# Kernel optimization log

Measured on AMD Instinct MI355X. Metric: run time of the kernel, lower is better.

Reference implementation:

```python
import jax, jax.numpy as jnp
import numpy as np

SCALE = 56          # descriptor spatial size (self.scale)
K_POS = 3           # positives: softmin over 3 nearest prototypes


def setup_inputs() -> dict:
    key = jax.random.key(0)
    k1, k2, k3 = jax.random.split(key, 3)
    B, DIM, H, W_ = 4, 1792, SCALE, SCALE
    P = 3136  # num_prototypes
    p = jax.random.normal(k1, (B, DIM, H, W_), dtype=jnp.float32)
    W = jax.random.normal(k2, (DIM, DIM), dtype=jnp.float32) * (1.0 / np.sqrt(DIM))
    b = jnp.zeros((DIM,), dtype=jnp.float32)
    C = jax.random.normal(k3, (DIM, P), dtype=jnp.float32) * (1.0 / np.sqrt(DIM))
    return {"p": p, "W": W, "b": b, "C": C}


def reference(p, W, b, C):
    B, DIM, H, Wd = p.shape
    # Descriptor: 1x1 conv (CoordConv2d without coords), no sigmoid, no avg-pool
    phi = jnp.einsum('bchw,dc->bdhw', p, W) + b[None, :, None, None]
    # b c h w -> b (h w) c
    phi_p = jnp.transpose(phi.reshape(B, DIM, H * Wd), (0, 2, 1))  # [B, HW, D]
    # squared-distance trick: ||a||^2 + ||c||^2 - 2 a.c
    features = jnp.sum(phi_p * phi_p, axis=2, keepdims=True)       # [B, HW, 1]
    centers = jnp.sum(C * C, axis=0, keepdims=True)                # [1, P]
    f_c = 2.0 * jnp.matmul(phi_p, C)                               # [B, HW, P]
    dist = jnp.sqrt(features + centers - f_c)                      # [B, HW, P]
    # k smallest distances (ascending)
    d = -jax.lax.top_k(-dist, K_POS)[0]                            # [B, HW, K]
    # softmin weight of the nearest prototype times its distance
    w0 = jax.nn.softmax(-d, axis=-1)[:, :, 0]
    score_flat = (w0 * d[:, :, 0])[:, :, None]                     # [B, HW, 1]
    # b (h w) c -> b c h w
    score = jnp.transpose(score_flat.reshape(B, H, Wd, 1), (0, 3, 1, 2))
    return score
```

## Files before the change

### kernel.cpp

```cpp
#include <hip/hip_runtime.h>
#include <hip/hip_bf16.h>
#include <cfloat>

#define BATCH 4
#define DIMC 1792
#define HWSZ 3136
#define NPROT 3136
#define NPAD 3200
#define MROWS 12544

typedef unsigned short u16;
typedef unsigned int u32;
using bf16x8 = __attribute__((ext_vector_type(8))) short;
using f32x4  = __attribute__((ext_vector_type(4))) float;

__device__ __forceinline__ float bf2f(u32 u) { return __uint_as_float(u << 16); }
__device__ __forceinline__ u16 f2bf(float x) {
    __hip_bfloat16 h = __float2bfloat16(x);
    return *reinterpret_cast<u16*>(&h);
}

__device__ __forceinline__ void gload_lds16(const u16* g, u16* l) {
    __builtin_amdgcn_global_load_lds(
        (const __attribute__((address_space(1))) void*)g,
        (__attribute__((address_space(3))) void*)l, 16, 0, 0);
}

__device__ __forceinline__ void ins3(float v, float& t0, float& t1, float& t2) {
    if (v < t2) {
        if (v < t1) {
            t2 = t1;
            if (v < t0) { t1 = t0; t0 = v; }
            else        { t1 = v; }
        } else {
            t2 = v;
        }
    }
}

__global__ void pack_p_kernel(const float* __restrict__ p, u16* __restrict__ Pbf) {
    __shared__ float tile[32][33];
    int hw0 = blockIdx.x * 32, c0 = blockIdx.y * 32, b = blockIdx.z;
    int tx = threadIdx.x, ty = threadIdx.y;
#pragma unroll
    for (int j = 0; j < 32; j += 8)
        tile[ty + j][tx] = p[((size_t)(b * DIMC + c0 + ty + j)) * HWSZ + hw0 + tx];
    __syncthreads();
#pragma unroll
    for (int j = 0; j < 32; j += 8) {
        int r = b * HWSZ + hw0 + ty + j;
        Pbf[(size_t)r * DIMC + c0 + tx] = f2bf(tile[tx][ty + j]);
    }
}

__global__ void pack_w_kernel(const float* __restrict__ W, u16* __restrict__ Wbf) {
    size_t i = (size_t)(blockIdx.x * 256 + threadIdx.x) * 4;
    float4 v = *(const float4*)(W + i);
    ushort4 o;
    o.x = f2bf(v.x); o.y = f2bf(v.y); o.z = f2bf(v.z); o.w = f2bf(v.w);
    *(ushort4*)(Wbf + i) = o;
}

__global__ void pack_c_kernel(const float* __restrict__ C, u16* __restrict__ CTbf) {
    __shared__ float tile[32][33];
    int j0 = blockIdx.x * 32, d0 = blockIdx.y * 32;
    int tx = threadIdx.x, ty = threadIdx.y;
#pragma unroll
    for (int jj = 0; jj < 32; jj += 8)
        tile[ty + jj][tx] = C[(size_t)(d0 + ty + jj) * NPROT + j0 + tx];
    __syncthreads();
#pragma unroll
    for (int jj = 0; jj < 32; jj += 8)
        CTbf[(size_t)(j0 + ty + jj) * DIMC + d0 + tx] = f2bf(tile[tx][ty + jj]);
}

__global__ void cn_kernel(const float* __restrict__ C, float* __restrict__ cn) {
    int j  = blockIdx.x * 256 + threadIdx.x;
    int d0 = blockIdx.y * 128;
    if (j >= NPROT) return;
    float s = 0.f;
    for (int d = d0; d < d0 + 128; ++d) {
        float v = C[(size_t)d * NPROT + j];
        s += v * v;
    }
    atomicAdd(&cn[j], s);
}

template<bool BIAS>
__global__ __launch_bounds__(256) void gemm_kernel(
    const u16* __restrict__ A,
    const u16* __restrict__ B,
    const float* __restrict__ bias,
    u16* __restrict__ out, int ldo)
{
    __shared__ __align__(16) u16 Als[128 * 32];
    __shared__ __align__(16) u16 Bls[128 * 32];
    const int tid  = threadIdx.x;
    const int wid  = tid >> 6;
    const int lane = tid & 63;
    const int r0 = blockIdx.x * 128;
    const int n0 = blockIdx.y * 128;

    const int srow = lane >> 2;
    const int sseg = (lane & 3) * 8;
    const u16* Ag = A + (size_t)(r0 + wid * 32 + srow) * DIMC + sseg;
    const u16* Bg = B + (size_t)(n0 + wid * 32 + srow) * DIMC + sseg;
    u16* AlsW = Als + wid * 1024;
    u16* BlsW = Bls + wid * 1024;

    const int wm = (wid >> 1) * 64;
    const int wn = (wid & 1) * 64;
    const int lrow = lane & 15;
    const int kseg = (lane >> 4) * 8;
    const int rsub = (lane >> 4) * 4;

    f32x4 acc[4][4];
#pragma unroll
    for (int m = 0; m < 4; ++m)
#pragma unroll
        for (int n = 0; n < 4; ++n)
            acc[m][n] = (f32x4){0.f, 0.f, 0.f, 0.f};

    for (int k0 = 0; k0 < DIMC; k0 += 32) {
        gload_lds16(Ag + k0,                      AlsW);
        gload_lds16(Ag + (size_t)16 * DIMC + k0,  AlsW + 512);
        gload_lds16(Bg + k0,                      BlsW);
        gload_lds16(Bg + (size_t)16 * DIMC + k0,  BlsW + 512);
        __syncthreads();
        bf16x8 af[4], bv[4];
#pragma unroll
        for (int m = 0; m < 4; ++m)
            af[m] = *(const bf16x8*)(Als + (wm + m * 16 + lrow) * 32 + kseg);
#pragma unroll
        for (int n = 0; n < 4; ++n)
            bv[n] = *(const bf16x8*)(Bls + (wn + n * 16 + lrow) * 32 + kseg);
#pragma unroll
        for (int m = 0; m < 4; ++m)
#pragma unroll
            for (int n = 0; n < 4; ++n)
                acc[m][n] = __builtin_amdgcn_mfma_f32_16x16x32_bf16(
                    af[m], bv[n], acc[m][n], 0, 0, 0);
        __syncthreads();
    }

#pragma unroll
    for (int n = 0; n < 4; ++n) {
        int col = n0 + wn + n * 16 + lrow;
        float bs = 0.f;
        if (BIAS) bs = bias[col];
#pragma unroll
        for (int m = 0; m < 4; ++m) {
            f32x4 v = acc[m][n];
#pragma unroll
            for (int i = 0; i < 4; ++i) {
                int row = r0 + wm + m * 16 + rsub + i;
                out[(size_t)row * ldo + col] = f2bf(v[i] + bs);
            }
        }
    }
}

__global__ void rn_kernel(const u16* __restrict__ phibf, float* __restrict__ rn) {
    int row  = blockIdx.x * 4 + (threadIdx.x >> 6);
    int lane = threadIdx.x & 63;
    const u16* pr = phibf + (size_t)row * DIMC;
    float s = 0.f;
#pragma unroll
    for (int it = 0; it < 7; ++it) {
        uint2 v = *(const uint2*)(pr + (it * 64 + lane) * 4);
        float f0 = bf2f(v.x & 0xffffu), f1 = bf2f(v.x >> 16);
        float f2 = bf2f(v.y & 0xffffu), f3 = bf2f(v.y >> 16);
        s += f0 * f0 + f1 * f1 + f2 * f2 + f3 * f3;
    }
#pragma unroll
    for (int off = 32; off > 0; off >>= 1) s += __shfl_down(s, off);
    if (lane == 0) rn[row] = s;
}

__global__ void top3_final_kernel(const u16* __restrict__ fc,
                                  const float* __restrict__ cn,
                                  const float* __restrict__ rn,
                                  float* __restrict__ out) {
    int row  = blockIdx.x * 4 + (threadIdx.x >> 6);
    int lane = threadIdx.x & 63;
    const u16* fr = fc + (size_t)row * NPAD;
    float t0 = FLT_MAX, t1 = FLT_MAX, t2 = FLT_MAX;
#pragma unroll
    for (int it = 0; it < 6; ++it) {
        int j0 = (it * 64 + lane) * 8;
        uint4 v = *(const uint4*)(fr + j0);
        u32 wd[4] = {v.x, v.y, v.z, v.w};
#pragma unroll
        for (int e = 0; e < 4; ++e) {
            float flo = bf2f(wd[e] & 0xffffu);
            float fhi = bf2f(wd[e] >> 16);
            ins3(cn[j0 + 2 * e]     - 2.f * flo, t0, t1, t2);
            ins3(cn[j0 + 2 * e + 1] - 2.f * fhi, t0, t1, t2);
        }
    }
    {
        int j = 3072 + lane;
        ins3(cn[j] - 2.f * bf2f((u32)fr[j]), t0, t1, t2);
    }
#pragma unroll
    for (int off = 32; off > 0; off >>= 1) {
        float s0 = __shfl_xor(t0, off);
        float s1 = __shfl_xor(t1, off);
        float s2 = __shfl_xor(t2, off);
        ins3(s0, t0, t1, t2);
        ins3(s1, t0, t1, t2);
        ins3(s2, t0, t1, t2);
    }
    if (lane == 0) {
        float rv = rn[row];
        float d0 = sqrtf(rv + t0), d1 = sqrtf(rv + t1), d2 = sqrtf(rv + t2);
        float w0 = 1.f / (1.f + expf(d0 - d1) + expf(d0 - d2));
        out[row] = w0 * d0;
    }
}

extern "C" void kernel_launch(void* const* d_in, const int* in_sizes, int n_in,
                              void* d_out, int out_size, void* d_ws, size_t ws_size,
                              hipStream_t stream) {
    const float* p    = (const float*)d_in[0];
    const float* W    = (const float*)d_in[1];
    const float* bias = (const float*)d_in[2];
    const float* C    = (const float*)d_in[3];
    float* out = (float*)d_out;

    char* w = (char*)d_ws;
    u16* Pbf   = (u16*)w;  w += (size_t)MROWS * DIMC * 2;
    u16* Wbf   = (u16*)w;  w += (size_t)DIMC * DIMC * 2;
    u16* CTbf  = (u16*)w;  w += (size_t)NPAD * DIMC * 2;
    u16* phibf = (u16*)w;  w += (size_t)MROWS * DIMC * 2;
    u16* fc    = (u16*)w;  w += (size_t)MROWS * NPAD * 2;
    float* cn  = (float*)w; w += (size_t)NPROT * 4;
    float* rn  = (float*)w;

    hipMemsetAsync(cn, 0, NPROT * sizeof(float), stream);

    pack_p_kernel<<<dim3(HWSZ / 32, DIMC / 32, BATCH), dim3(32, 8), 0, stream>>>(p, Pbf);
    pack_w_kernel<<<(DIMC * DIMC / 4) / 256, 256, 0, stream>>>(W, Wbf);
    pack_c_kernel<<<dim3(NPROT / 32, DIMC / 32), dim3(32, 8), 0, stream>>>(C, CTbf);
    cn_kernel<<<dim3((NPROT + 255) / 256, DIMC / 128), 256, 0, stream>>>(C, cn);

    gemm_kernel<true><<<dim3(MROWS / 128, DIMC / 128), 256, 0, stream>>>(
        Pbf, Wbf, bias, phibf, DIMC);
    rn_kernel<<<MROWS / 4, 256, 0, stream>>>(phibf, rn);
    gemm_kernel<false><<<dim3(MROWS / 128, NPAD / 128), 256, 0, stream>>>(
        phibf, CTbf, nullptr, fc, NPAD);
    top3_final_kernel<<<MROWS / 4, 256, 0, stream>>>(fc, cn, rn, out);
}
```

Baseline: 647.6 us.

## Use 256x256 double-buffered swizzled GEMM tiles and fuse norm kernels

Replaces the 128x128 single-buffered GEMM with a 512-thread 256x256 tile kernel that double-buffers LDS, prefetches the next K-tile while computing, and XOR-swizzles LDS rows to cut bank conflicts. The centroid-norm computation is folded into the C pack kernel and the row-norm kernel into the top-3 kernel, removing two launches and extra passes over memory. The pack_p stores become vectorized, and NPAD grows to a multiple of 256. The large LDS footprint limits occupancy to one block per CU.

```diff
diff --git a/kernel.cpp b/kernel.cpp
--- a/kernel.cpp
+++ b/kernel.cpp
@@ -6,8 +6,9 @@
 #define DIMC 1792
 #define HWSZ 3136
 #define NPROT 3136
-#define NPAD 3200
+#define NPAD 3328
 #define MROWS 12544
+#define NKT 28
 
 typedef unsigned short u16;
 typedef unsigned int u32;
@@ -41,16 +42,21 @@
 __global__ void pack_p_kernel(const float* __restrict__ p, u16* __restrict__ Pbf) {
     __shared__ float tile[32][33];
     int hw0 = blockIdx.x * 32, c0 = blockIdx.y * 32, b = blockIdx.z;
-    int tx = threadIdx.x, ty = threadIdx.y;
+    int tid = threadIdx.x;
+    int tx = tid & 31, ty = tid >> 5;
 #pragma unroll
     for (int j = 0; j < 32; j += 8)
         tile[ty + j][tx] = p[((size_t)(b * DIMC + c0 + ty + j)) * HWSZ + hw0 + tx];
     __syncthreads();
-#pragma unroll
-    for (int j = 0; j < 32; j += 8) {
-        int r = b * HWSZ + hw0 + ty + j;
-        Pbf[(size_t)r * DIMC + c0 + tx] = f2bf(tile[tx][ty + j]);
-    }
+    int hwl = tid >> 3;
+    int c4  = (tid & 7) * 4;
+    int r = b * HWSZ + hw0 + hwl;
+    ushort4 o;
+    o.x = f2bf(tile[c4 + 0][hwl]);
+    o.y = f2bf(tile[c4 + 1][hwl]);
+    o.z = f2bf(tile[c4 + 2][hwl]);
+    o.w = f2bf(tile[c4 + 3][hwl]);
+    *(ushort4*)(Pbf + (size_t)r * DIMC + c0 + c4) = o;
 }
 
 __global__ void pack_w_kernel(const float* __restrict__ W, u16* __restrict__ Wbf) {
@@ -61,95 +67,119 @@
     *(ushort4*)(Wbf + i) = o;
 }
 
-__global__ void pack_c_kernel(const float* __restrict__ C, u16* __restrict__ CTbf) {
+__global__ void pack_c_kernel(const float* __restrict__ C, u16* __restrict__ CTbf,
+                              float* __restrict__ cn) {
     __shared__ float tile[32][33];
     int j0 = blockIdx.x * 32, d0 = blockIdx.y * 32;
-    int tx = threadIdx.x, ty = threadIdx.y;
+    int tid = threadIdx.x;
+    int tx = tid & 31, ty = tid >> 5;
 #pragma unroll
     for (int jj = 0; jj < 32; jj += 8)
         tile[ty + jj][tx] = C[(size_t)(d0 + ty + jj) * NPROT + j0 + tx];
     __syncthreads();
-#pragma unroll
-    for (int jj = 0; jj < 32; jj += 8)
-        CTbf[(size_t)(j0 + ty + jj) * DIMC + d0 + tx] = f2bf(tile[tx][ty + jj]);
-}
-
-__global__ void cn_kernel(const float* __restrict__ C, float* __restrict__ cn) {
-    int j  = blockIdx.x * 256 + threadIdx.x;
-    int d0 = blockIdx.y * 128;
-    if (j >= NPROT) return;
+    int jl = tid >> 3;
+    int d4 = (tid & 7) * 4;
     float s = 0.f;
-    for (int d = d0; d < d0 + 128; ++d) {
-        float v = C[(size_t)d * NPROT + j];
-        s += v * v;
-    }
-    atomicAdd(&cn[j], s);
+    ushort4 o;
+    {
+        float f0 = tile[d4 + 0][jl], f1 = tile[d4 + 1][jl];
+        float f2 = tile[d4 + 2][jl], f3 = tile[d4 + 3][jl];
+        o.x = f2bf(f0); o.y = f2bf(f1); o.z = f2bf(f2); o.w = f2bf(f3);
+        s = f0 * f0 + f1 * f1 + f2 * f2 + f3 * f3;
+    }
+    *(ushort4*)(CTbf + (size_t)(j0 + jl) * DIMC + d0 + d4) = o;
+#pragma unroll
+    for (int off = 1; off < 8; off <<= 1) s += __shfl_xor(s, off);
+    if ((tid & 7) == 0) atomicAdd(&cn[j0 + jl], s);
 }
 
 template<bool BIAS>
-__global__ __launch_bounds__(256) void gemm_kernel(
-    const u16* __restrict__ A,
-    const u16* __restrict__ B,
-    const float* __restrict__ bias,
-    u16* __restrict__ out, int ldo)
+__global__ __launch_bounds__(512, 2) void gemm8_kernel(
+    const u16* __restrict__ A, const u16* __restrict__ B,
+    const float* __restrict__ bias, u16* __restrict__ out, int ldo)
 {
-    __shared__ __align__(16) u16 Als[128 * 32];
-    __shared__ __align__(16) u16 Bls[128 * 32];
+    __shared__ __align__(16) u16 Als[4][256 * 32];
+    __shared__ __align__(16) u16 Bls[4][256 * 32];
     const int tid  = threadIdx.x;
     const int wid  = tid >> 6;
     const int lane = tid & 63;
-    const int r0 = blockIdx.x * 128;
-    const int n0 = blockIdx.y * 128;
-
-    const int srow = lane >> 2;
-    const int sseg = (lane & 3) * 8;
-    const u16* Ag = A + (size_t)(r0 + wid * 32 + srow) * DIMC + sseg;
-    const u16* Bg = B + (size_t)(n0 + wid * 32 + srow) * DIMC + sseg;
-    u16* AlsW = Als + wid * 1024;
-    u16* BlsW = Bls + wid * 1024;
-
-    const int wm = (wid >> 1) * 64;
-    const int wn = (wid & 1) * 64;
+    const int r0 = blockIdx.x * 256;
+    const int n0 = blockIdx.y * 256;
+
+    const int wm = (wid >> 2) * 128;
+    const int wn = (wid & 3) * 64;
     const int lrow = lane & 15;
-    const int kseg = (lane >> 4) * 8;
     const int rsub = (lane >> 4) * 4;
-
-    f32x4 acc[4][4];
-#pragma unroll
-    for (int m = 0; m < 4; ++m)
+    const int kxor = (((lane >> 4) ^ (lrow & 3))) * 8;
+
+    const int f1 = tid,       r1 = f1 >> 2, g1 = ((f1 & 3) ^ (r1 & 3)) * 8;
+    const int f2 = tid + 512, r2 = f2 >> 2, g2 = ((f2 & 3) ^ (r2 & 3)) * 8;
+    const u16* Abase = A + (size_t)r0 * DIMC;
+    const u16* Bbase = B + (size_t)n0 * DIMC;
+    const int wofs = wid * 512;
+
+    f32x4 acc[8][4];
+#pragma unroll
+    for (int m = 0; m < 8; ++m)
 #pragma unroll
         for (int n = 0; n < 4; ++n)
             acc[m][n] = (f32x4){0.f, 0.f, 0.f, 0.f};
 
-    for (int k0 = 0; k0 < DIMC; k0 += 32) {
-        gload_lds16(Ag + k0,                      AlsW);
-        gload_lds16(Ag + (size_t)16 * DIMC + k0,  AlsW + 512);
-        gload_lds16(Bg + k0,                      BlsW);
-        gload_lds16(Bg + (size_t)16 * DIMC + k0,  BlsW + 512);
-        __syncthreads();
-        bf16x8 af[4], bv[4];
-#pragma unroll
-        for (int m = 0; m < 4; ++m)
-            af[m] = *(const bf16x8*)(Als + (wm + m * 16 + lrow) * 32 + kseg);
-#pragma unroll
-        for (int n = 0; n < 4; ++n)
-            bv[n] = *(const bf16x8*)(Bls + (wn + n * 16 + lrow) * 32 + kseg);
-#pragma unroll
-        for (int m = 0; m < 4; ++m)
+    auto STAGE = [&](int t, int bf) {
+        const u16* At = Abase + t * 64;
+        const u16* Bt = Bbase + t * 64;
+#pragma unroll
+        for (int ks = 0; ks < 2; ++ks) {
+            gload_lds16(At + (size_t)r1 * DIMC + ks * 32 + g1, &Als[bf * 2 + ks][wofs]);
+            gload_lds16(At + (size_t)r2 * DIMC + ks * 32 + g2, &Als[bf * 2 + ks][4096 + wofs]);
+            gload_lds16(Bt + (size_t)r1 * DIMC + ks * 32 + g1, &Bls[bf * 2 + ks][wofs]);
+            gload_lds16(Bt + (size_t)r2 * DIMC + ks * 32 + g2, &Bls[bf * 2 + ks][4096 + wofs]);
+        }
+    };
+
+    auto COMPUTE = [&](int bf) {
+#pragma unroll
+        for (int ks = 0; ks < 2; ++ks) {
+            const u16* ab = Als[bf * 2 + ks];
+            const u16* bb = Bls[bf * 2 + ks];
+            bf16x8 af[8], bv[4];
+#pragma unroll
+            for (int m = 0; m < 8; ++m)
+                af[m] = *(const bf16x8*)(ab + (wm + m * 16 + lrow) * 32 + kxor);
 #pragma unroll
             for (int n = 0; n < 4; ++n)
-                acc[m][n] = __builtin_amdgcn_mfma_f32_16x16x32_bf16(
-                    af[m], bv[n], acc[m][n], 0, 0, 0);
-        __syncthreads();
-    }
+                bv[n] = *(const bf16x8*)(bb + (wn + n * 16 + lrow) * 32 + kxor);
+#pragma unroll
+            for (int m = 0; m < 8; ++m)
+#pragma unroll
+                for (int n = 0; n < 4; ++n)
+                    acc[m][n] = __builtin_amdgcn_mfma_f32_16x16x32_bf16(
+                        af[m], bv[n], acc[m][n], 0, 0, 0);
+        }
+    };
+
+    STAGE(0, 0);
+    for (int t = 0; t < NKT - 1; ++t) {
+        int bf = t & 1;
+        STAGE(t + 1, bf ^ 1);
+        __builtin_amdgcn_sched_barrier(0);
+        asm volatile("s_waitcnt vmcnt(8)" ::: "memory");
+        __builtin_amdgcn_s_barrier();
+        __builtin_amdgcn_sched_barrier(0);
+        COMPUTE(bf);
+        __builtin_amdgcn_sched_barrier(0);
+        __builtin_amdgcn_s_barrier();
+    }
+    asm volatile("s_waitcnt vmcnt(0)" ::: "memory");
+    __builtin_amdgcn_s_barrier();
+    COMPUTE((NKT - 1) & 1);
 
 #pragma unroll
     for (int n = 0; n < 4; ++n) {
         int col = n0 + wn + n * 16 + lrow;
-        float bs = 0.f;
-        if (BIAS) bs = bias[col];
-#pragma unroll
-        for (int m = 0; m < 4; ++m) {
+        float bs = BIAS ? bias[col] : 0.f;
+#pragma unroll
+        for (int m = 0; m < 8; ++m) {
             f32x4 v = acc[m][n];
 #pragma unroll
             for (int i = 0; i < 4; ++i) {
@@ -160,9 +190,13 @@
     }
 }
 
-__global__ void rn_kernel(const u16* __restrict__ phibf, float* __restrict__ rn) {
+__global__ void top3_final_kernel(const u16* __restrict__ fc,
+                                  const u16* __restrict__ phibf,
+                                  const float* __restrict__ cn,
+                                  float* __restrict__ out) {
     int row  = blockIdx.x * 4 + (threadIdx.x >> 6);
     int lane = threadIdx.x & 63;
+
     const u16* pr = phibf + (size_t)row * DIMC;
     float s = 0.f;
 #pragma unroll
@@ -174,15 +208,7 @@
     }
 #pragma unroll
     for (int off = 32; off > 0; off >>= 1) s += __shfl_down(s, off);
-    if (lane == 0) rn[row] = s;
-}
-
-__global__ void top3_final_kernel(const u16* __restrict__ fc,
-                                  const float* __restrict__ cn,
-                                  const float* __restrict__ rn,
-                                  float* __restrict__ out) {
-    int row  = blockIdx.x * 4 + (threadIdx.x >> 6);
-    int lane = threadIdx.x & 63;
+
     const u16* fr = fc + (size_t)row * NPAD;
     float t0 = FLT_MAX, t1 = FLT_MAX, t2 = FLT_MAX;
 #pragma unroll
@@ -212,7 +238,7 @@
         ins3(s2, t0, t1, t2);
     }
     if (lane == 0) {
-        float rv = rn[row];
+        float rv = s;
         float d0 = sqrtf(rv + t0), d1 = sqrtf(rv + t1), d2 = sqrtf(rv + t2);
         float w0 = 1.f / (1.f + expf(d0 - d1) + expf(d0 - d2));
         out[row] = w0 * d0;
@@ -234,20 +260,17 @@
     u16* CTbf  = (u16*)w;  w += (size_t)NPAD * DIMC * 2;
     u16* phibf = (u16*)w;  w += (size_t)MROWS * DIMC * 2;
     u16* fc    = (u16*)w;  w += (size_t)MROWS * NPAD * 2;
-    float* cn  = (float*)w; w += (size_t)NPROT * 4;
-    float* rn  = (float*)w;
+    float* cn  = (float*)w;
 
     hipMemsetAsync(cn, 0, NPROT * sizeof(float), stream);
 
-    pack_p_kernel<<<dim3(HWSZ / 32, DIMC / 32, BATCH), dim3(32, 8), 0, stream>>>(p, Pbf);
+    pack_p_kernel<<<dim3(HWSZ / 32, DIMC / 32, BATCH), 256, 0, stream>>>(p, Pbf);
     pack_w_kernel<<<(DIMC * DIMC / 4) / 256, 256, 0, stream>>>(W, Wbf);
-    pack_c_kernel<<<dim3(NPROT / 32, DIMC / 32), dim3(32, 8), 0, stream>>>(C, CTbf);
-    cn_kernel<<<dim3((NPROT + 255) / 256, DIMC / 128), 256, 0, stream>>>(C, cn);
-
-    gemm_kernel<true><<<dim3(MROWS / 128, DIMC / 128), 256, 0, stream>>>(
+    pack_c_kernel<<<dim3(NPROT / 32, DIMC / 32), 256, 0, stream>>>(C, CTbf, cn);
+
+    gemm8_kernel<true><<<dim3(MROWS / 256, DIMC / 256), 512, 0, stream>>>(
         Pbf, Wbf, bias, phibf, DIMC);
-    rn_kernel<<<MROWS / 4, 256, 0, stream>>>(phibf, rn);
-    gemm_kernel<false><<<dim3(MROWS / 128, NPAD / 128), 256, 0, stream>>>(
+    gemm8_kernel<false><<<dim3(MROWS / 256, NPAD / 256), 512, 0, stream>>>(
         phibf, CTbf, nullptr, fc, NPAD);
-    top3_final_kernel<<<MROWS / 4, 256, 0, stream>>>(fc, cn, rn, out);
-}
+    top3_final_kernel<<<MROWS / 4, 256, 0, stream>>>(fc, phibf, cn, out);
+}
```

New measurement: 681.8 us. 5.3% more time.
